# Optimization experiments

Hardware: AMD Instinct MI355X
Metric: run time of the kernel (lower is better)

The kernel has to match this reference:

```python
import jax, jax.numpy as jnp
import numpy as np

MAX_ITERS = 30
NDIM = 3
TAU = 1.0 / (2.0 * NDIM)  # skimage Chambolle step size


def _grad(u, ax):
    # forward difference along ax, zero at the last slice (skimage convention)
    g = jnp.diff(u, axis=ax)
    pad = [(0, 0)] * u.ndim
    pad[ax] = (0, 1)
    return jnp.pad(g, pad)


def _div(p):
    # adjoint of _grad: d[ax] = shift_forward(p[ax]) - p[ax]
    d = jnp.zeros_like(p[0])
    for ax in range(NDIM):
        pa = p[ax]
        sl = [slice(None)] * NDIM
        sl[ax] = slice(0, -1)
        pad = [(0, 0)] * NDIM
        pad[ax] = (1, 0)
        d = d + jnp.pad(pa[tuple(sl)], pad) - pa
    return d


def tv_chambolle_nd(image, weight):
    # Chambolle projection algorithm (skimage _denoise_tv_chambolle_nd), fixed iters.
    def step(p, _):
        out = image + _div(p)
        g = jnp.stack([_grad(out, ax) for ax in range(NDIM)], axis=0)  # (3,B,T,F)
        norm = jnp.sqrt(jnp.sum(g * g, axis=0, keepdims=True))
        norm = norm * (TAU / weight) + 1.0
        return (p - TAU * g) / norm, None

    p0 = jnp.zeros((NDIM,) + image.shape, image.dtype)
    # iteration i returns out built from p after i updates; after max_iters loop
    # iterations the returned `out` used p updated (max_iters-1) times.
    p, _ = jax.lax.scan(jax.checkpoint(step), p0, None, length=MAX_ITERS - 1)
    return image + _div(p)


def setup_inputs() -> dict:
    key = jax.random.key(0)
    kx, kl, kb = jax.random.split(key, 3)
    x = jax.random.normal(kx, (8, 2048, 128), dtype=jnp.float32)
    # lambdas has a non-neg constraint; keep it strictly positive
    lambdas = jax.random.uniform(kl, (1, 1), dtype=jnp.float32) * 0.1 + 0.05
    b = jax.random.normal(kb, (1, 1, 128), dtype=jnp.float32) * 0.01
    return {"x": x, "lambdas": lambdas, "b": b}


def reference(x, lambdas, b):
    out = tv_chambolle_nd(x.astype(jnp.float32), lambdas)
    out = out + b  # use_bias=True; activation=None
    return out
```

## Files before the change

kernel.cpp:

```cpp
#include <hip/hip_runtime.h>


#define BB 8
#define TT 2048
#define FF 128
#define NV (BB*TT*FF)
#define SB (TT*FF)
#define ST FF
#define RR 8
#define NBLK (TT/RR)
#define HH 4
#define EE (RR + 2*HH)
#define GR (EE/2)

constexpr float TAU = 1.0f / 6.0f;

__device__ __forceinline__ float4 ld4(const float* p) { return *reinterpret_cast<const float4*>(p); }
__device__ __forceinline__ void st4(float* p, const float4& v) { *reinterpret_cast<float4*>(p) = v; }
__device__ __forceinline__ float4 shfl_up4(float4 v, int d) {
    return make_float4(__shfl_up(v.x, d), __shfl_up(v.y, d), __shfl_up(v.z, d), __shfl_up(v.w, d));
}
__device__ __forceinline__ float4 shfl_dn4(float4 v, int d) {
    return make_float4(__shfl_down(v.x, d), __shfl_down(v.y, d), __shfl_down(v.z, d), __shfl_down(v.w, d));
}
__device__ __forceinline__ float4 sub4(const float4& a, const float4& b) {
    return make_float4(a.x - b.x, a.y - b.y, a.z - b.z, a.w - b.w);
}
__device__ __forceinline__ float4 f4z() { return make_float4(0.f, 0.f, 0.f, 0.f); }
__device__ __forceinline__ float4 nbvec(const float4& gB, const float4& gT, const float4& gF, float s) {
    float4 nb; float q;
    q = gB.x * gB.x + gT.x * gT.x + gF.x * gF.x;
    nb.x = __builtin_amdgcn_rcpf(fmaf(__builtin_amdgcn_sqrtf(q), s, 1.f));
    q = gB.y * gB.y + gT.y * gT.y + gF.y * gF.y;
    nb.y = __builtin_amdgcn_rcpf(fmaf(__builtin_amdgcn_sqrtf(q), s, 1.f));
    q = gB.z * gB.z + gT.z * gT.z + gF.z * gF.z;
    nb.z = __builtin_amdgcn_rcpf(fmaf(__builtin_amdgcn_sqrtf(q), s, 1.f));
    q = gB.w * gB.w + gT.w * gT.w + gF.w * gF.w;
    nb.w = __builtin_amdgcn_rcpf(fmaf(__builtin_amdgcn_sqrtf(q), s, 1.f));
    return nb;
}

struct ConeShared {
    float p2b[EE][4][8];
    float outx[EE][4][8];
    float4 p1if[256];
    float4 oif[256];
};

template<int RG>
__device__ __forceinline__ void publish_p(int k, float4 (&P1)[GR], float4 (&P2)[GR],
                                          ConeShared& sh, int c, int b, int fg, int w) {
    if (fg == 7) {
        #pragma unroll
        for (int le = 0; le < GR; ++le) {
            const int e = RG * GR + le;
            if (e >= k && e < EE - k) sh.p2b[e][w][b] = P2[le].w;
        }
    }
    if (RG == 0) sh.p1if[c] = P1[GR - 1];
}

template<int RG, bool ELO, bool EHI>
__device__ __forceinline__ void phase_out(
    int k, const float4 (&Xr)[GR],
    float4 (&P0)[GR], float4 (&P1)[GR], float4 (&P2)[GR], float4 (&O)[GR],
    ConeShared& sh, int c, int b, int fg, int w, int f0, int tb) {
    #pragma unroll
    for (int le = 0; le < GR; ++le) {
        const int e = RG * GR + le;
        if (e < k + 1 || e >= EE - k) continue;
        const int t = tb + e;
        if ((ELO && t < 0) || (EHI && t >= TT)) continue;
        const float4 X = Xr[le];
        float4 o;
        o.x = X.x - P0[le].x - P1[le].x - P2[le].x;
        o.y = X.y - P0[le].y - P1[le].y - P2[le].y + P2[le].x;
        o.z = X.z - P0[le].z - P1[le].z - P2[le].z + P2[le].y;
        o.w = X.w - P0[le].w - P1[le].w - P2[le].w + P2[le].z;
        float4 h0 = shfl_up4(P0[le], 1);
        if (b > 0) { o.x += h0.x; o.y += h0.y; o.z += h0.z; o.w += h0.w; }
        float4 pm1 = (le > 0) ? P1[le - 1] : sh.p1if[c];
        if (!ELO || t > 0) { o.x += pm1.x; o.y += pm1.y; o.z += pm1.z; o.w += pm1.w; }
        float pw = __shfl_up(P2[le].w, 8);
        if (fg == 0) pw = (w > 0) ? sh.p2b[e][w - 1][b] : 0.0f;
        if (f0 > 0) o.x += pw;
        O[le] = o;
        if (fg == 0) sh.outx[e][w][b] = o.x;
    }
}

template<int RG, bool ELO, bool EHI>
__device__ __forceinline__ void phase_upd(
    int k, float4 (&P0)[GR], float4 (&P1)[GR], float4 (&P2)[GR], float4 (&O)[GR],
    ConeShared& sh, int c, int b, int fg, int w, int f0, int tb, float s) {
    #pragma unroll
    for (int le = 0; le < GR; ++le) {
        const int e = RG * GR + le;
        if (e < k + 1 || e > EE - 2 - k) continue;
        const int t = tb + e;
        if ((ELO && t < 0) || (EHI && t >= TT)) continue;
        const float4 cc = O[le];
        float4 on = (le < GR - 1) ? O[le + 1] : sh.oif[c];
        float4 gT = f4z();
        if (!EHI || t < TT - 1) gT = sub4(on, cc);
        const float4 nB = shfl_dn4(cc, 1);
        float4 gB = f4z();
        if (b < BB - 1) gB = sub4(nB, cc);
        float nxx = __shfl_down(cc.x, 8);
        if (fg == 7) nxx = (w < 3) ? sh.outx[e][w + 1][b] : 0.0f;
        float4 gF;
        gF.x = cc.y - cc.x;
        gF.y = cc.z - cc.y;
        gF.z = cc.w - cc.z;
        gF.w = (f0 < FF - 4) ? (nxx - cc.w) : 0.f;
        const float4 nb = nbvec(gB, gT, gF, s);
        P0[le].x = fmaf(-TAU, gB.x, P0[le].x) * nb.x;
        P0[le].y = fmaf(-TAU, gB.y, P0[le].y) * nb.y;
        P0[le].z = fmaf(-TAU, gB.z, P0[le].z) * nb.z;
        P0[le].w = fmaf(-TAU, gB.w, P0[le].w) * nb.w;
        P1[le].x = fmaf(-TAU, gT.x, P1[le].x) * nb.x;
        P1[le].y = fmaf(-TAU, gT.y, P1[le].y) * nb.y;
        P1[le].z = fmaf(-TAU, gT.z, P1[le].z) * nb.z;
        P1[le].w = fmaf(-TAU, gT.w, P1[le].w) * nb.w;
        P2[le].x = fmaf(-TAU, gF.x, P2[le].x) * nb.x;
        P2[le].y = fmaf(-TAU, gF.y, P2[le].y) * nb.y;
        P2[le].z = fmaf(-TAU, gF.z, P2[le].z) * nb.z;
        P2[le].w = fmaf(-TAU, gF.w, P2[le].w) * nb.w;
    }
}

template<bool ELO, bool EHI>
__device__ __forceinline__ void cone_run(
    const float4 (&Xr)[GR],
    float4 (&P0)[GR], float4 (&P1)[GR], float4 (&P2)[GR], float4 (&O)[GR],
    ConeShared& sh, int rg, int c, int b, int fg, int w, int f0, int tb, float s) {
    #pragma unroll
    for (int k = 0; k < HH; ++k) {
        if (rg == 0) publish_p<0>(k, P1, P2, sh, c, b, fg, w);
        else         publish_p<1>(k, P1, P2, sh, c, b, fg, w);
        __syncthreads();
        if (rg == 0) phase_out<0, ELO, EHI>(k, Xr, P0, P1, P2, O, sh, c, b, fg, w, f0, tb);
        else         phase_out<1, ELO, EHI>(k, Xr, P0, P1, P2, O, sh, c, b, fg, w, f0, tb);
        if (rg == 1) sh.oif[c] = O[0];
        __syncthreads();
        if (rg == 0) phase_upd<0, ELO, EHI>(k, P0, P1, P2, O, sh, c, b, fg, w, f0, tb, s);
        else         phase_upd<1, ELO, EHI>(k, P0, P1, P2, O, sh, c, b, fg, w, f0, tb, s);
    }
}

template<bool ELO, bool EHI>
__device__ __forceinline__ void tb_main(
    const float* __restrict__ x, const float* __restrict__ pin, float* __restrict__ pout,
    ConeShared& sh, int rg, int c, int b, int fg, int w, int f0, int tb, int e0,
    int base, float s) {
    float4 P0[GR], P1[GR], P2[GR], O[GR], Xr[GR];
    #pragma unroll
    for (int le = 0; le < GR; ++le) {
        const int t = tb + e0 + le;
        if ((!ELO || t >= 0) && (!EHI || t < TT)) {
            const int v = base + t * ST;
            P0[le] = ld4(pin + v);
            P1[le] = ld4(pin + NV + v);
            P2[le] = ld4(pin + 2 * NV + v);
            Xr[le] = ld4(x + v);
        } else {
            P0[le] = f4z(); P1[le] = f4z(); P2[le] = f4z(); Xr[le] = f4z();
        }
        O[le] = f4z();
    }
    cone_run<ELO, EHI>(Xr, P0, P1, P2, O, sh, rg, c, b, fg, w, f0, tb, s);
    #pragma unroll
    for (int le = 0; le < GR; ++le) {
        const int e = e0 + le;
        if (e >= HH && e < HH + RR) {
            const int v = base + (tb + e) * ST;
            st4(pout + v, P0[le]);
            st4(pout + NV + v, P1[le]);
            st4(pout + 2 * NV + v, P2[le]);
        }
    }
}

__global__ __launch_bounds__(512, 2)
void k_tb(const float* __restrict__ x, const float* __restrict__ pin,
          float* __restrict__ pout, const float* __restrict__ lam) {
    __shared__ ConeShared sh;
    const int tid = threadIdx.x;
    const int blk = blockIdx.x;
    const int rg  = tid >> 8;
    const int c   = tid & 255;
    const int b   = tid & 7;
    const int fg  = (tid >> 3) & 7;
    const int w   = (tid >> 6) & 3;
    const int f0  = w * 32 + fg * 4;
    const int tb  = blk * RR - HH;
    const int e0  = rg * GR;
    const int base = b * SB + f0;
    const float s = TAU / lam[0];
    if (blk == 0 || blk == NBLK - 1)
        tb_main<true, true>(x, pin, pout, sh, rg, c, b, fg, w, f0, tb, e0, base, s);
    else
        tb_main<false, false>(x, pin, pout, sh, rg, c, b, fg, w, f0, tb, e0, base, s);
}

template<bool ELO, bool EHI>
__device__ __forceinline__ void tb_first_main(
    const float* __restrict__ x, float* __restrict__ pout,
    ConeShared& sh, int rg, int c, int b, int fg, int w, int f0, int tb, int e0,
    int base, float s) {
    float4 P0[GR], P1[GR], P2[GR], O[GR], Xr[GR], XH;
    #pragma unroll
    for (int le = 0; le < GR; ++le) {
        const int t = tb + e0 + le;
        Xr[le] = ((!ELO || t >= 0) && (!EHI || t < TT)) ? ld4(x + base + t * ST) : f4z();
        O[le] = f4z();
    }
    {
        const int t = tb + e0 + GR;
        XH = ((!ELO || t >= 0) && (!EHI || t < TT)) ? ld4(x + base + t * ST) : f4z();
    }
    #pragma unroll
    for (int le = 0; le < GR; ++le) {
        const int t = tb + e0 + le;
        if ((!ELO || t >= 0) && (!EHI || t < TT)) {
            const float4 cc = Xr[le];
            float4 nxt = (le < GR - 1) ? Xr[le + 1] : XH;
            float4 gT = f4z();
            if (!EHI || t < TT - 1) gT = sub4(nxt, cc);
            const float4 nB = shfl_dn4(cc, 1);
            float4 gB = f4z();
            if (b < BB - 1) gB = sub4(nB, cc);
            float4 gF;
            gF.x = cc.y - cc.x;
            gF.y = cc.z - cc.y;
            gF.z = cc.w - cc.z;
            gF.w = (f0 < FF - 4) ? (x[base + t * ST + 4] - cc.w) : 0.f;
            const float4 nb = nbvec(gB, gT, gF, s);
            P0[le] = make_float4(-TAU * gB.x * nb.x, -TAU * gB.y * nb.y,
                                 -TAU * gB.z * nb.z, -TAU * gB.w * nb.w);
            P1[le] = make_float4(-TAU * gT.x * nb.x, -TAU * gT.y * nb.y,
                                 -TAU * gT.z * nb.z, -TAU * gT.w * nb.w);
            P2[le] = make_float4(-TAU * gF.x * nb.x, -TAU * gF.y * nb.y,
                                 -TAU * gF.z * nb.z, -TAU * gF.w * nb.w);
        } else {
            P0[le] = f4z(); P1[le] = f4z(); P2[le] = f4z();
        }
    }
    cone_run<ELO, EHI>(Xr, P0, P1, P2, O, sh, rg, c, b, fg, w, f0, tb, s);
    #pragma unroll
    for (int le = 0; le < GR; ++le) {
        const int e = e0 + le;
        if (e >= HH && e < HH + RR) {
            const int v = base + (tb + e) * ST;
            st4(pout + v, P0[le]);
            st4(pout + NV + v, P1[le]);
            st4(pout + 2 * NV + v, P2[le]);
        }
    }
}

__global__ __launch_bounds__(512, 2)
void k_tb_first(const float* __restrict__ x, float* __restrict__ pout,
                const float* __restrict__ lam) {
    __shared__ ConeShared sh;
    const int tid = threadIdx.x;
    const int blk = blockIdx.x;
    const int rg  = tid >> 8;
    const int c   = tid & 255;
    const int b   = tid & 7;
    const int fg  = (tid >> 3) & 7;
    const int w   = (tid >> 6) & 3;
    const int f0  = w * 32 + fg * 4;
    const int tb  = blk * RR - HH;
    const int e0  = rg * GR;
    const int base = b * SB + f0;
    const float s = TAU / lam[0];
    if (blk == 0 || blk == NBLK - 1)
        tb_first_main<true, true>(x, pout, sh, rg, c, b, fg, w, f0, tb, e0, base, s);
    else
        tb_first_main<false, false>(x, pout, sh, rg, c, b, fg, w, f0, tb, e0, base, s);
}

__global__ __launch_bounds__(256)
void k_final(const float* __restrict__ x, const float* __restrict__ pin,
             const float* __restrict__ bias, float* __restrict__ out) {
    const int gid = blockIdx.x * 256 + threadIdx.x;
    const int v = gid * 4;
    const int f0 = v & (FF - 1);
    const int t = (v >> 7) & (TT - 1);
    const int b = v >> 18;
    const float* p0 = pin;
    const float* p1 = pin + NV;
    const float* p2 = pin + 2 * NV;
    float4 X = ld4(x + v);
    float4 a0 = ld4(p0 + v), a1 = ld4(p1 + v), a2 = ld4(p2 + v);
    float ox = X.x - a0.x - a1.x - a2.x;
    float oy = X.y - a0.y - a1.y - a2.y + a2.x;
    float oz = X.z - a0.z - a1.z - a2.z + a2.y;
    float ow = X.w - a0.w - a1.w - a2.w + a2.z;
    if (b > 0) { float4 h = ld4(p0 + v - SB); ox += h.x; oy += h.y; oz += h.z; ow += h.w; }
    if (t > 0) { float4 h = ld4(p1 + v - ST); ox += h.x; oy += h.y; oz += h.z; ow += h.w; }
    if (f0 > 0) ox += p2[v - 1];
    float4 bi = ld4(bias + f0);
    st4(out + v, make_float4(ox + bi.x, oy + bi.y, oz + bi.z, ow + bi.w));
}

extern "C" void kernel_launch(void* const* d_in, const int* in_sizes, int n_in,
                              void* d_out, int out_size, void* d_ws, size_t ws_size,
                              hipStream_t stream) {
    const float* x    = (const float*)d_in[0];
    const float* lam  = (const float*)d_in[1];
    const float* bias = (const float*)d_in[2];
    float* out = (float*)d_out;

    float* pA = (float*)d_ws;
    float* pB = pA + 3 * NV;

    k_tb_first<<<NBLK, 512, 0, stream>>>(x, pA, lam);
    float* pin = pA;
    float* pout = pB;
    for (int i = 0; i < 6; ++i) {
        k_tb<<<NBLK, 512, 0, stream>>>(x, pin, pout, lam);
        float* tmp = pin; pin = pout; pout = tmp;
    }
    k_final<<<NV / 1024, 256, 0, stream>>>(x, pin, bias, out);
}
```

Baseline: 270.5 us.

## Drop second barrier per cone step by recomputing halo outputs redundantly

Each thread group now computes the neighbouring halo output values it needs (the next time row, and the x component of the next feature chunk) from published p values and extra x loads, so out values no longer have to be exchanged through shared memory. This removes one __syncthreads per cone iteration, and double-buffered shared arrays indexed by iteration parity avoid write-after-read hazards. The cost is extra shared-memory traffic, redundant arithmetic, more registers and a larger shared footprint, which could lower occupancy.

```diff
diff --git a/kernel.cpp b/kernel.cpp
--- a/kernel.cpp
+++ b/kernel.cpp
@@ -41,29 +41,51 @@
 }
 
 struct ConeShared {
-    float p2b[EE][4][8];
-    float outx[EE][4][8];
-    float4 p1if[256];
-    float4 oif[256];
+    float4 pIF0[2][256];
+    float4 pIF1[2][256];
+    float4 pIF2[2][256];
+    float4 p1if[2][256];
+    float  px0[2][EE][32];
+    float  px1[2][EE][32];
+    float  px2[2][EE][32];
+    float  p2b[2][EE][32];
 };
 
 template<int RG>
-__device__ __forceinline__ void publish_p(int k, float4 (&P1)[GR], float4 (&P2)[GR],
-                                          ConeShared& sh, int c, int b, int fg, int w) {
+__device__ __forceinline__ void publish(int par, float4 (&P0)[GR], float4 (&P1)[GR],
+                                        float4 (&P2)[GR], ConeShared& sh,
+                                        int c, int b, int fg, int w) {
+    if (RG == 1) {
+        sh.pIF0[par][c] = P0[0];
+        sh.pIF1[par][c] = P1[0];
+        sh.pIF2[par][c] = P2[0];
+    } else {
+        sh.p1if[par][c] = P1[GR - 1];
+    }
+    const int cw = w * 8 + b;
+    if (fg == 0) {
+        #pragma unroll
+        for (int le = 0; le < GR; ++le) {
+            const int e = RG * GR + le;
+            sh.px0[par][e][cw] = P0[le].x;
+            sh.px1[par][e][cw] = P1[le].x;
+            sh.px2[par][e][cw] = P2[le].x;
+        }
+    }
     if (fg == 7) {
         #pragma unroll
         for (int le = 0; le < GR; ++le) {
             const int e = RG * GR + le;
-            if (e >= k && e < EE - k) sh.p2b[e][w][b] = P2[le].w;
-        }
-    }
-    if (RG == 0) sh.p1if[c] = P1[GR - 1];
+            sh.p2b[par][e][cw] = P2[le].w;
+        }
+    }
 }
 
 template<int RG, bool ELO, bool EHI>
 __device__ __forceinline__ void phase_out(
-    int k, const float4 (&Xr)[GR],
+    int k, int par, const float4 (&Xr)[GR], const float4& XH, const float (&XH4)[GR],
     float4 (&P0)[GR], float4 (&P1)[GR], float4 (&P2)[GR], float4 (&O)[GR],
+    float (&ohx)[GR], float4& OH,
     ConeShared& sh, int c, int b, int fg, int w, int f0, int tb) {
     #pragma unroll
     for (int le = 0; le < GR; ++le) {
@@ -79,20 +101,46 @@
         o.w = X.w - P0[le].w - P1[le].w - P2[le].w + P2[le].z;
         float4 h0 = shfl_up4(P0[le], 1);
         if (b > 0) { o.x += h0.x; o.y += h0.y; o.z += h0.z; o.w += h0.w; }
-        float4 pm1 = (le > 0) ? P1[le - 1] : sh.p1if[c];
+        float4 pm1 = (le > 0) ? P1[le - 1] : sh.p1if[par][c];
         if (!ELO || t > 0) { o.x += pm1.x; o.y += pm1.y; o.z += pm1.z; o.w += pm1.w; }
         float pw = __shfl_up(P2[le].w, 8);
-        if (fg == 0) pw = (w > 0) ? sh.p2b[e][w - 1][b] : 0.0f;
+        if (fg == 0) pw = (w > 0) ? sh.p2b[par][e][(w - 1) * 8 + b] : 0.0f;
         if (f0 > 0) o.x += pw;
         O[le] = o;
-        if (fg == 0) sh.outx[e][w][b] = o.x;
+        if (fg == 7 && w < 3) {
+            const int cw = (w + 1) * 8 + b;
+            float hx = XH4[le] - sh.px0[par][e][cw] - sh.px1[par][e][cw] - sh.px2[par][e][cw]
+                     + P2[le].w;
+            if (b > 0) hx += sh.px0[par][e][cw - 1];
+            if (!ELO || t > 0) hx += sh.px1[par][e - 1][cw];
+            ohx[le] = hx;
+        }
+    }
+    if (RG == 0) {
+        const float4 q0 = sh.pIF0[par][c];
+        const float4 q1 = sh.pIF1[par][c];
+        const float4 q2 = sh.pIF2[par][c];
+        float4 o;
+        o.x = XH.x - q0.x - q1.x - q2.x;
+        o.y = XH.y - q0.y - q1.y - q2.y + q2.x;
+        o.z = XH.z - q0.z - q1.z - q2.z + q2.y;
+        o.w = XH.w - q0.w - q1.w - q2.w + q2.z;
+        if (b > 0) {
+            const float4 h = sh.pIF0[par][c - 1];
+            o.x += h.x; o.y += h.y; o.z += h.z; o.w += h.w;
+        }
+        o.x += P1[GR - 1].x; o.y += P1[GR - 1].y;
+        o.z += P1[GR - 1].z; o.w += P1[GR - 1].w;
+        if (f0 > 0) o.x += sh.pIF2[par][c - 8].w;
+        OH = o;
     }
 }
 
 template<int RG, bool ELO, bool EHI>
 __device__ __forceinline__ void phase_upd(
     int k, float4 (&P0)[GR], float4 (&P1)[GR], float4 (&P2)[GR], float4 (&O)[GR],
-    ConeShared& sh, int c, int b, int fg, int w, int f0, int tb, float s) {
+    const float (&ohx)[GR], const float4& OH,
+    int b, int fg, int w, int f0, int tb, float s) {
     #pragma unroll
     for (int le = 0; le < GR; ++le) {
         const int e = RG * GR + le;
@@ -100,14 +148,14 @@
         const int t = tb + e;
         if ((ELO && t < 0) || (EHI && t >= TT)) continue;
         const float4 cc = O[le];
-        float4 on = (le < GR - 1) ? O[le + 1] : sh.oif[c];
+        const float4 on = (le < GR - 1) ? O[le + 1] : OH;
         float4 gT = f4z();
         if (!EHI || t < TT - 1) gT = sub4(on, cc);
         const float4 nB = shfl_dn4(cc, 1);
         float4 gB = f4z();
         if (b < BB - 1) gB = sub4(nB, cc);
         float nxx = __shfl_down(cc.x, 8);
-        if (fg == 7) nxx = (w < 3) ? sh.outx[e][w + 1][b] : 0.0f;
+        if (fg == 7) nxx = (w < 3) ? ohx[le] : 0.0f;
         float4 gF;
         gF.x = cc.y - cc.x;
         gF.y = cc.z - cc.y;
@@ -131,20 +179,26 @@
 
 template<bool ELO, bool EHI>
 __device__ __forceinline__ void cone_run(
-    const float4 (&Xr)[GR],
+    const float4 (&Xr)[GR], const float4& XH, const float (&XH4)[GR],
     float4 (&P0)[GR], float4 (&P1)[GR], float4 (&P2)[GR], float4 (&O)[GR],
     ConeShared& sh, int rg, int c, int b, int fg, int w, int f0, int tb, float s) {
+    float ohx[GR];
+    #pragma unroll
+    for (int le = 0; le < GR; ++le) ohx[le] = 0.f;
+    float4 OH = f4z();
     #pragma unroll
     for (int k = 0; k < HH; ++k) {
-        if (rg == 0) publish_p<0>(k, P1, P2, sh, c, b, fg, w);
-        else         publish_p<1>(k, P1, P2, sh, c, b, fg, w);
+        const int par = k & 1;
+        if (rg == 0) publish<0>(par, P0, P1, P2, sh, c, b, fg, w);
+        else         publish<1>(par, P0, P1, P2, sh, c, b, fg, w);
         __syncthreads();
-        if (rg == 0) phase_out<0, ELO, EHI>(k, Xr, P0, P1, P2, O, sh, c, b, fg, w, f0, tb);
-        else         phase_out<1, ELO, EHI>(k, Xr, P0, P1, P2, O, sh, c, b, fg, w, f0, tb);
-        if (rg == 1) sh.oif[c] = O[0];
-        __syncthreads();
-        if (rg == 0) phase_upd<0, ELO, EHI>(k, P0, P1, P2, O, sh, c, b, fg, w, f0, tb, s);
-        else         phase_upd<1, ELO, EHI>(k, P0, P1, P2, O, sh, c, b, fg, w, f0, tb, s);
+        if (rg == 0) {
+            phase_out<0, ELO, EHI>(k, par, Xr, XH, XH4, P0, P1, P2, O, ohx, OH, sh, c, b, fg, w, f0, tb);
+            phase_upd<0, ELO, EHI>(k, P0, P1, P2, O, ohx, OH, b, fg, w, f0, tb, s);
+        } else {
+            phase_out<1, ELO, EHI>(k, par, Xr, XH, XH4, P0, P1, P2, O, ohx, OH, sh, c, b, fg, w, f0, tb);
+            phase_upd<1, ELO, EHI>(k, P0, P1, P2, O, ohx, OH, b, fg, w, f0, tb, s);
+        }
     }
 }
 
@@ -154,10 +208,12 @@
     ConeShared& sh, int rg, int c, int b, int fg, int w, int f0, int tb, int e0,
     int base, float s) {
     float4 P0[GR], P1[GR], P2[GR], O[GR], Xr[GR];
+    float  XH4[GR];
     #pragma unroll
     for (int le = 0; le < GR; ++le) {
         const int t = tb + e0 + le;
-        if ((!ELO || t >= 0) && (!EHI || t < TT)) {
+        const bool v_ok = (!ELO || t >= 0) && (!EHI || t < TT);
+        if (v_ok) {
             const int v = base + t * ST;
             P0[le] = ld4(pin + v);
             P1[le] = ld4(pin + NV + v);
@@ -166,9 +222,12 @@
         } else {
             P0[le] = f4z(); P1[le] = f4z(); P2[le] = f4z(); Xr[le] = f4z();
         }
+        XH4[le] = (fg == 7 && w < 3 && v_ok) ? x[base + t * ST + 4] : 0.f;
         O[le] = f4z();
     }
-    cone_run<ELO, EHI>(Xr, P0, P1, P2, O, sh, rg, c, b, fg, w, f0, tb, s);
+    float4 XH = f4z();
+    if (rg == 0) XH = ld4(x + base + (tb + GR) * ST);
+    cone_run<ELO, EHI>(Xr, XH, XH4, P0, P1, P2, O, sh, rg, c, b, fg, w, f0, tb, s);
     #pragma unroll
     for (int le = 0; le < GR; ++le) {
         const int e = e0 + le;
@@ -208,25 +267,29 @@
     const float* __restrict__ x, float* __restrict__ pout,
     ConeShared& sh, int rg, int c, int b, int fg, int w, int f0, int tb, int e0,
     int base, float s) {
-    float4 P0[GR], P1[GR], P2[GR], O[GR], Xr[GR], XH;
+    float4 P0[GR], P1[GR], P2[GR], O[GR], Xr[GR], XHa;
+    float  XH4[GR];
     #pragma unroll
     for (int le = 0; le < GR; ++le) {
         const int t = tb + e0 + le;
-        Xr[le] = ((!ELO || t >= 0) && (!EHI || t < TT)) ? ld4(x + base + t * ST) : f4z();
+        const bool v_ok = (!ELO || t >= 0) && (!EHI || t < TT);
+        Xr[le] = v_ok ? ld4(x + base + t * ST) : f4z();
+        XH4[le] = (fg == 7 && w < 3 && v_ok) ? x[base + t * ST + 4] : 0.f;
         O[le] = f4z();
     }
     {
         const int t = tb + e0 + GR;
-        XH = ((!ELO || t >= 0) && (!EHI || t < TT)) ? ld4(x + base + t * ST) : f4z();
+        const bool v_ok = (!ELO || t >= 0) && (t < TT);
+        XHa = v_ok ? ld4(x + base + t * ST) : f4z();
     }
     #pragma unroll
     for (int le = 0; le < GR; ++le) {
         const int t = tb + e0 + le;
         if ((!ELO || t >= 0) && (!EHI || t < TT)) {
             const float4 cc = Xr[le];
-            float4 nxt = (le < GR - 1) ? Xr[le + 1] : XH;
+            const float4 nxt = (le < GR - 1) ? Xr[le + 1] : XHa;
             float4 gT = f4z();
-            if (!EHI || t < TT - 1) gT = sub4(nxt, cc);
+            if (t < TT - 1) gT = sub4(nxt, cc);
             const float4 nB = shfl_dn4(cc, 1);
             float4 gB = f4z();
             if (b < BB - 1) gB = sub4(nB, cc);
@@ -246,7 +309,7 @@
             P0[le] = f4z(); P1[le] = f4z(); P2[le] = f4z();
         }
     }
-    cone_run<ELO, EHI>(Xr, P0, P1, P2, O, sh, rg, c, b, fg, w, f0, tb, s);
+    cone_run<ELO, EHI>(Xr, XHa, XH4, P0, P1, P2, O, sh, rg, c, b, fg, w, f0, tb, s);
     #pragma unroll
     for (int le = 0; le < GR; ++le) {
         const int e = e0 + le;
```

After: 296.9 us. 9.8% more time.

## Fuse final divergence and bias into last temporal-blocked iteration kernel

Applied to the files above, without the earlier changes.

Replaces the separate final elementwise kernel and one mid temporal-block launch with a k_last kernel. It runs the last four iterations on a wider 18-row window, then computes the output divergence plus bias in-register and writes the result directly. The change also skips loading P0, P2 and X for the first halo row, which only needs P1. This removes one full pass over the p buffers and x, at the cost of more registers and a larger halo in the last kernel.

```diff
diff --git a/kernel.cpp b/kernel.cpp
--- a/kernel.cpp
+++ b/kernel.cpp
@@ -9,9 +9,6 @@
 #define ST FF
 #define RR 8
 #define NBLK (TT/RR)
-#define HH 4
-#define EE (RR + 2*HH)
-#define GR (EE/2)
 
 constexpr float TAU = 1.0f / 6.0f;
 
@@ -41,34 +38,36 @@
 }
 
 struct ConeShared {
-    float p2b[EE][4][8];
-    float outx[EE][4][8];
+    float p2b[18][4][8];
+    float outx[18][4][8];
     float4 p1if[256];
     float4 oif[256];
 };
 
-template<int RG>
-__device__ __forceinline__ void publish_p(int k, float4 (&P1)[GR], float4 (&P2)[GR],
-                                          ConeShared& sh, int c, int b, int fg, int w) {
+template<int EEt, int RG>
+__device__ __forceinline__ void publish(int k, float4 (&P1)[EEt/2], float4 (&P2)[EEt/2],
+                                        ConeShared& sh, int c, int b, int fg, int w) {
+    constexpr int GRt = EEt / 2;
     if (fg == 7) {
         #pragma unroll
-        for (int le = 0; le < GR; ++le) {
-            const int e = RG * GR + le;
-            if (e >= k && e < EE - k) sh.p2b[e][w][b] = P2[le].w;
-        }
-    }
-    if (RG == 0) sh.p1if[c] = P1[GR - 1];
-}
-
-template<int RG, bool ELO, bool EHI>
+        for (int le = 0; le < GRt; ++le) {
+            const int e = RG * GRt + le;
+            if (e >= k && e < EEt - k) sh.p2b[e][w][b] = P2[le].w;
+        }
+    }
+    if (RG == 0) sh.p1if[c] = P1[GRt - 1];
+}
+
+template<int EEt, int RG, bool ELO, bool EHI>
 __device__ __forceinline__ void phase_out(
-    int k, const float4 (&Xr)[GR],
-    float4 (&P0)[GR], float4 (&P1)[GR], float4 (&P2)[GR], float4 (&O)[GR],
+    int k, const float4 (&Xr)[EEt/2],
+    float4 (&P0)[EEt/2], float4 (&P1)[EEt/2], float4 (&P2)[EEt/2], float4 (&O)[EEt/2],
     ConeShared& sh, int c, int b, int fg, int w, int f0, int tb) {
-    #pragma unroll
-    for (int le = 0; le < GR; ++le) {
-        const int e = RG * GR + le;
-        if (e < k + 1 || e >= EE - k) continue;
+    constexpr int GRt = EEt / 2;
+    #pragma unroll
+    for (int le = 0; le < GRt; ++le) {
+        const int e = RG * GRt + le;
+        if (e < k + 1 || e >= EEt - k) continue;
         const int t = tb + e;
         if ((ELO && t < 0) || (EHI && t >= TT)) continue;
         const float4 X = Xr[le];
@@ -82,25 +81,26 @@
         float4 pm1 = (le > 0) ? P1[le - 1] : sh.p1if[c];
         if (!ELO || t > 0) { o.x += pm1.x; o.y += pm1.y; o.z += pm1.z; o.w += pm1.w; }
         float pw = __shfl_up(P2[le].w, 8);
-        if (fg == 0) pw = (w > 0) ? sh.p2b[e][w - 1][b] : 0.0f;
+        if (fg == 0) pw = (w > 0) ? sh.p2b[e][(w - 1)][b] : 0.0f;
         if (f0 > 0) o.x += pw;
         O[le] = o;
         if (fg == 0) sh.outx[e][w][b] = o.x;
     }
 }
 
-template<int RG, bool ELO, bool EHI>
+template<int EEt, int RG, bool ELO, bool EHI>
 __device__ __forceinline__ void phase_upd(
-    int k, float4 (&P0)[GR], float4 (&P1)[GR], float4 (&P2)[GR], float4 (&O)[GR],
+    int k, float4 (&P0)[EEt/2], float4 (&P1)[EEt/2], float4 (&P2)[EEt/2], float4 (&O)[EEt/2],
     ConeShared& sh, int c, int b, int fg, int w, int f0, int tb, float s) {
-    #pragma unroll
-    for (int le = 0; le < GR; ++le) {
-        const int e = RG * GR + le;
-        if (e < k + 1 || e > EE - 2 - k) continue;
+    constexpr int GRt = EEt / 2;
+    #pragma unroll
+    for (int le = 0; le < GRt; ++le) {
+        const int e = RG * GRt + le;
+        if (e < k + 1 || e > EEt - 2 - k) continue;
         const int t = tb + e;
         if ((ELO && t < 0) || (EHI && t >= TT)) continue;
         const float4 cc = O[le];
-        float4 on = (le < GR - 1) ? O[le + 1] : sh.oif[c];
+        const float4 on = (le < GRt - 1) ? O[le + 1] : sh.oif[c];
         float4 gT = f4z();
         if (!EHI || t < TT - 1) gT = sub4(on, cc);
         const float4 nB = shfl_dn4(cc, 1);
@@ -129,50 +129,55 @@
     }
 }
 
-template<bool ELO, bool EHI>
+template<int EEt, int HHt, bool ELO, bool EHI>
 __device__ __forceinline__ void cone_run(
-    const float4 (&Xr)[GR],
-    float4 (&P0)[GR], float4 (&P1)[GR], float4 (&P2)[GR], float4 (&O)[GR],
+    const float4 (&Xr)[EEt/2],
+    float4 (&P0)[EEt/2], float4 (&P1)[EEt/2], float4 (&P2)[EEt/2], float4 (&O)[EEt/2],
     ConeShared& sh, int rg, int c, int b, int fg, int w, int f0, int tb, float s) {
     #pragma unroll
-    for (int k = 0; k < HH; ++k) {
-        if (rg == 0) publish_p<0>(k, P1, P2, sh, c, b, fg, w);
-        else         publish_p<1>(k, P1, P2, sh, c, b, fg, w);
+    for (int k = 0; k < HHt; ++k) {
+        if (rg == 0) publish<EEt, 0>(k, P1, P2, sh, c, b, fg, w);
+        else         publish<EEt, 1>(k, P1, P2, sh, c, b, fg, w);
         __syncthreads();
-        if (rg == 0) phase_out<0, ELO, EHI>(k, Xr, P0, P1, P2, O, sh, c, b, fg, w, f0, tb);
-        else         phase_out<1, ELO, EHI>(k, Xr, P0, P1, P2, O, sh, c, b, fg, w, f0, tb);
+        if (rg == 0) phase_out<EEt, 0, ELO, EHI>(k, Xr, P0, P1, P2, O, sh, c, b, fg, w, f0, tb);
+        else         phase_out<EEt, 1, ELO, EHI>(k, Xr, P0, P1, P2, O, sh, c, b, fg, w, f0, tb);
         if (rg == 1) sh.oif[c] = O[0];
         __syncthreads();
-        if (rg == 0) phase_upd<0, ELO, EHI>(k, P0, P1, P2, O, sh, c, b, fg, w, f0, tb, s);
-        else         phase_upd<1, ELO, EHI>(k, P0, P1, P2, O, sh, c, b, fg, w, f0, tb, s);
+        if (rg == 0) phase_upd<EEt, 0, ELO, EHI>(k, P0, P1, P2, O, sh, c, b, fg, w, f0, tb, s);
+        else         phase_upd<EEt, 1, ELO, EHI>(k, P0, P1, P2, O, sh, c, b, fg, w, f0, tb, s);
     }
 }
 
 template<bool ELO, bool EHI>
-__device__ __forceinline__ void tb_main(
+__device__ __forceinline__ void mid_main(
     const float* __restrict__ x, const float* __restrict__ pin, float* __restrict__ pout,
     ConeShared& sh, int rg, int c, int b, int fg, int w, int f0, int tb, int e0,
     int base, float s) {
-    float4 P0[GR], P1[GR], P2[GR], O[GR], Xr[GR];
-    #pragma unroll
-    for (int le = 0; le < GR; ++le) {
+    constexpr int GRt = 8;
+    float4 P0[GRt], P1[GRt], P2[GRt], O[GRt], Xr[GRt];
+    #pragma unroll
+    for (int le = 0; le < GRt; ++le) {
         const int t = tb + e0 + le;
-        if ((!ELO || t >= 0) && (!EHI || t < TT)) {
+        const bool ok = (!ELO || t >= 0) && (!EHI || t < TT);
+        const bool trim = (rg == 0 && le == 0);
+        if (ok) {
             const int v = base + t * ST;
-            P0[le] = ld4(pin + v);
             P1[le] = ld4(pin + NV + v);
-            P2[le] = ld4(pin + 2 * NV + v);
-            Xr[le] = ld4(x + v);
+            if (!trim) {
+                P0[le] = ld4(pin + v);
+                P2[le] = ld4(pin + 2 * NV + v);
+                Xr[le] = ld4(x + v);
+            } else { P0[le] = f4z(); P2[le] = f4z(); Xr[le] = f4z(); }
         } else {
             P0[le] = f4z(); P1[le] = f4z(); P2[le] = f4z(); Xr[le] = f4z();
         }
         O[le] = f4z();
     }
-    cone_run<ELO, EHI>(Xr, P0, P1, P2, O, sh, rg, c, b, fg, w, f0, tb, s);
-    #pragma unroll
-    for (int le = 0; le < GR; ++le) {
+    cone_run<16, 4, ELO, EHI>(Xr, P0, P1, P2, O, sh, rg, c, b, fg, w, f0, tb, s);
+    #pragma unroll
+    for (int le = 0; le < GRt; ++le) {
         const int e = e0 + le;
-        if (e >= HH && e < HH + RR) {
+        if (e >= 4 && e < 12) {
             const int v = base + (tb + e) * ST;
             st4(pout + v, P0[le]);
             st4(pout + NV + v, P1[le]);
@@ -182,8 +187,8 @@
 }
 
 __global__ __launch_bounds__(512, 2)
-void k_tb(const float* __restrict__ x, const float* __restrict__ pin,
-          float* __restrict__ pout, const float* __restrict__ lam) {
+void k_mid(const float* __restrict__ x, const float* __restrict__ pin,
+           float* __restrict__ pout, const float* __restrict__ lam) {
     __shared__ ConeShared sh;
     const int tid = threadIdx.x;
     const int blk = blockIdx.x;
@@ -193,40 +198,43 @@
     const int fg  = (tid >> 3) & 7;
     const int w   = (tid >> 6) & 3;
     const int f0  = w * 32 + fg * 4;
-    const int tb  = blk * RR - HH;
-    const int e0  = rg * GR;
+    const int tb  = blk * RR - 4;
+    const int e0  = rg * 8;
     const int base = b * SB + f0;
     const float s = TAU / lam[0];
     if (blk == 0 || blk == NBLK - 1)
-        tb_main<true, true>(x, pin, pout, sh, rg, c, b, fg, w, f0, tb, e0, base, s);
+        mid_main<true, true>(x, pin, pout, sh, rg, c, b, fg, w, f0, tb, e0, base, s);
     else
-        tb_main<false, false>(x, pin, pout, sh, rg, c, b, fg, w, f0, tb, e0, base, s);
+        mid_main<false, false>(x, pin, pout, sh, rg, c, b, fg, w, f0, tb, e0, base, s);
 }
 
 template<bool ELO, bool EHI>
-__device__ __forceinline__ void tb_first_main(
+__device__ __forceinline__ void first_main(
     const float* __restrict__ x, float* __restrict__ pout,
     ConeShared& sh, int rg, int c, int b, int fg, int w, int f0, int tb, int e0,
     int base, float s) {
-    float4 P0[GR], P1[GR], P2[GR], O[GR], Xr[GR], XH;
-    #pragma unroll
-    for (int le = 0; le < GR; ++le) {
+    constexpr int GRt = 8;
+    float4 P0[GRt], P1[GRt], P2[GRt], O[GRt], Xr[GRt], XHa;
+    #pragma unroll
+    for (int le = 0; le < GRt; ++le) {
         const int t = tb + e0 + le;
-        Xr[le] = ((!ELO || t >= 0) && (!EHI || t < TT)) ? ld4(x + base + t * ST) : f4z();
+        const bool ok = (!ELO || t >= 0) && (!EHI || t < TT);
+        Xr[le] = ok ? ld4(x + base + t * ST) : f4z();
         O[le] = f4z();
     }
     {
-        const int t = tb + e0 + GR;
-        XH = ((!ELO || t >= 0) && (!EHI || t < TT)) ? ld4(x + base + t * ST) : f4z();
-    }
-    #pragma unroll
-    for (int le = 0; le < GR; ++le) {
+        const int t = tb + e0 + GRt;
+        const bool ok = (!ELO || t >= 0) && (t < TT);
+        XHa = ok ? ld4(x + base + t * ST) : f4z();
+    }
+    #pragma unroll
+    for (int le = 0; le < GRt; ++le) {
         const int t = tb + e0 + le;
         if ((!ELO || t >= 0) && (!EHI || t < TT)) {
             const float4 cc = Xr[le];
-            float4 nxt = (le < GR - 1) ? Xr[le + 1] : XH;
+            const float4 nxt = (le < GRt - 1) ? Xr[le + 1] : XHa;
             float4 gT = f4z();
-            if (!EHI || t < TT - 1) gT = sub4(nxt, cc);
+            if (t < TT - 1) gT = sub4(nxt, cc);
             const float4 nB = shfl_dn4(cc, 1);
             float4 gB = f4z();
             if (b < BB - 1) gB = sub4(nB, cc);
@@ -246,11 +254,11 @@
             P0[le] = f4z(); P1[le] = f4z(); P2[le] = f4z();
         }
     }
-    cone_run<ELO, EHI>(Xr, P0, P1, P2, O, sh, rg, c, b, fg, w, f0, tb, s);
-    #pragma unroll
-    for (int le = 0; le < GR; ++le) {
+    cone_run<16, 4, ELO, EHI>(Xr, P0, P1, P2, O, sh, rg, c, b, fg, w, f0, tb, s);
+    #pragma unroll
+    for (int le = 0; le < GRt; ++le) {
         const int e = e0 + le;
-        if (e >= HH && e < HH + RR) {
+        if (e >= 4 && e < 12) {
             const int v = base + (tb + e) * ST;
             st4(pout + v, P0[le]);
             st4(pout + NV + v, P1[le]);
@@ -260,8 +268,8 @@
 }
 
 __global__ __launch_bounds__(512, 2)
-void k_tb_first(const float* __restrict__ x, float* __restrict__ pout,
-                const float* __restrict__ lam) {
+void k_first(const float* __restrict__ x, float* __restrict__ pout,
+             const float* __restrict__ lam) {
     __shared__ ConeShared sh;
     const int tid = threadIdx.x;
     const int blk = blockIdx.x;
@@ -271,38 +279,91 @@
     const int fg  = (tid >> 3) & 7;
     const int w   = (tid >> 6) & 3;
     const int f0  = w * 32 + fg * 4;
-    const int tb  = blk * RR - HH;
-    const int e0  = rg * GR;
+    const int tb  = blk * RR - 4;
+    const int e0  = rg * 8;
     const int base = b * SB + f0;
     const float s = TAU / lam[0];
     if (blk == 0 || blk == NBLK - 1)
-        tb_first_main<true, true>(x, pout, sh, rg, c, b, fg, w, f0, tb, e0, base, s);
+        first_main<true, true>(x, pout, sh, rg, c, b, fg, w, f0, tb, e0, base, s);
     else
-        tb_first_main<false, false>(x, pout, sh, rg, c, b, fg, w, f0, tb, e0, base, s);
-}
-
-__global__ __launch_bounds__(256)
-void k_final(const float* __restrict__ x, const float* __restrict__ pin,
-             const float* __restrict__ bias, float* __restrict__ out) {
-    const int gid = blockIdx.x * 256 + threadIdx.x;
-    const int v = gid * 4;
-    const int f0 = v & (FF - 1);
-    const int t = (v >> 7) & (TT - 1);
-    const int b = v >> 18;
-    const float* p0 = pin;
-    const float* p1 = pin + NV;
-    const float* p2 = pin + 2 * NV;
-    float4 X = ld4(x + v);
-    float4 a0 = ld4(p0 + v), a1 = ld4(p1 + v), a2 = ld4(p2 + v);
-    float ox = X.x - a0.x - a1.x - a2.x;
-    float oy = X.y - a0.y - a1.y - a2.y + a2.x;
-    float oz = X.z - a0.z - a1.z - a2.z + a2.y;
-    float ow = X.w - a0.w - a1.w - a2.w + a2.z;
-    if (b > 0) { float4 h = ld4(p0 + v - SB); ox += h.x; oy += h.y; oz += h.z; ow += h.w; }
-    if (t > 0) { float4 h = ld4(p1 + v - ST); ox += h.x; oy += h.y; oz += h.z; ow += h.w; }
-    if (f0 > 0) ox += p2[v - 1];
-    float4 bi = ld4(bias + f0);
-    st4(out + v, make_float4(ox + bi.x, oy + bi.y, oz + bi.z, ow + bi.w));
+        first_main<false, false>(x, pout, sh, rg, c, b, fg, w, f0, tb, e0, base, s);
+}
+
+template<bool ELO, bool EHI>
+__device__ __forceinline__ void last_main(
+    const float* __restrict__ x, const float* __restrict__ pin,
+    const float* __restrict__ bias, float* __restrict__ out,
+    ConeShared& sh, int rg, int c, int b, int fg, int w, int f0, int tb, int e0,
+    int base, float s) {
+    constexpr int GRt = 9;
+    float4 P0[GRt], P1[GRt], P2[GRt], O[GRt], Xr[GRt];
+    #pragma unroll
+    for (int le = 0; le < GRt; ++le) {
+        const int t = tb + e0 + le;
+        const bool ok = (!ELO || t >= 0) && (!EHI || t < TT);
+        const bool trim = (rg == 0 && le == 0);
+        if (ok) {
+            const int v = base + t * ST;
+            P1[le] = ld4(pin + NV + v);
+            if (!trim) {
+                P0[le] = ld4(pin + v);
+                P2[le] = ld4(pin + 2 * NV + v);
+                Xr[le] = ld4(x + v);
+            } else { P0[le] = f4z(); P2[le] = f4z(); Xr[le] = f4z(); }
+        } else {
+            P0[le] = f4z(); P1[le] = f4z(); P2[le] = f4z(); Xr[le] = f4z();
+        }
+        O[le] = f4z();
+    }
+    cone_run<18, 4, ELO, EHI>(Xr, P0, P1, P2, O, sh, rg, c, b, fg, w, f0, tb, s);
+    if (rg == 0) publish<18, 0>(4, P1, P2, sh, c, b, fg, w);
+    else         publish<18, 1>(4, P1, P2, sh, c, b, fg, w);
+    __syncthreads();
+    const float4 bi = ld4(bias + f0);
+    #pragma unroll
+    for (int le = 0; le < GRt; ++le) {
+        const int e = e0 + le;
+        if (e < 5 || e >= 13) continue;
+        const int t = tb + e;
+        const float4 X = Xr[le];
+        float4 o;
+        o.x = X.x - P0[le].x - P1[le].x - P2[le].x;
+        o.y = X.y - P0[le].y - P1[le].y - P2[le].y + P2[le].x;
+        o.z = X.z - P0[le].z - P1[le].z - P2[le].z + P2[le].y;
+        o.w = X.w - P0[le].w - P1[le].w - P2[le].w + P2[le].z;
+        float4 h0 = shfl_up4(P0[le], 1);
+        if (b > 0) { o.x += h0.x; o.y += h0.y; o.z += h0.z; o.w += h0.w; }
+        float4 pm1 = (le > 0) ? P1[le - 1] : sh.p1if[c];
+        if (!ELO || t > 0) { o.x += pm1.x; o.y += pm1.y; o.z += pm1.z; o.w += pm1.w; }
+        float pw = __shfl_up(P2[le].w, 8);
+        if (fg == 0) pw = (w > 0) ? sh.p2b[e][w - 1][b] : 0.0f;
+        if (f0 > 0) o.x += pw;
+        o.x += bi.x; o.y += bi.y; o.z += bi.z; o.w += bi.w;
+        st4(out + base + t * ST, o);
+    }
+}
+
+__global__ __launch_bounds__(512, 2)
+void k_last(const float* __restrict__ x, const float* __restrict__ pin,
+            const float* __restrict__ bias, float* __restrict__ out,
+            const float* __restrict__ lam) {
+    __shared__ ConeShared sh;
+    const int tid = threadIdx.x;
+    const int blk = blockIdx.x;
+    const int rg  = tid >> 8;
+    const int c   = tid & 255;
+    const int b   = tid & 7;
+    const int fg  = (tid >> 3) & 7;
+    const int w   = (tid >> 6) & 3;
+    const int f0  = w * 32 + fg * 4;
+    const int tb  = blk * RR - 5;
+    const int e0  = rg * 9;
+    const int base = b * SB + f0;
+    const float s = TAU / lam[0];
+    if (blk == 0 || blk == NBLK - 1)
+        last_main<true, true>(x, pin, bias, out, sh, rg, c, b, fg, w, f0, tb, e0, base, s);
+    else
+        last_main<false, false>(x, pin, bias, out, sh, rg, c, b, fg, w, f0, tb, e0, base, s);
 }
 
 extern "C" void kernel_launch(void* const* d_in, const int* in_sizes, int n_in,
@@ -316,12 +377,12 @@
     float* pA = (float*)d_ws;
     float* pB = pA + 3 * NV;
 
-    k_tb_first<<<NBLK, 512, 0, stream>>>(x, pA, lam);
+    k_first<<<NBLK, 512, 0, stream>>>(x, pA, lam);
     float* pin = pA;
     float* pout = pB;
-    for (int i = 0; i < 6; ++i) {
-        k_tb<<<NBLK, 512, 0, stream>>>(x, pin, pout, lam);
+    for (int i = 0; i < 5; ++i) {
+        k_mid<<<NBLK, 512, 0, stream>>>(x, pin, pout, lam);
         float* tmp = pin; pin = pout; pout = tmp;
     }
-    k_final<<<NV / 1024, 256, 0, stream>>>(x, pin, bias, out);
-}
+    k_last<<<NBLK, 512, 0, stream>>>(x, pin, bias, out, lam);
+}
```

Result: slower. 277.2 us (+2.5%).
